# Performance work log

Measured on AMD Instinct MI355X. Metric: run time of the kernel, lower is better.

The kernel has to match this reference:

```python
import jax, jax.numpy as jnp
import numpy as np

DIM = 1024
HID = 256
MAXT = 2048
B = 4
T = 2048


def setup_inputs() -> dict:
    key = jax.random.key(0)
    ks = jax.random.split(key, 10)
    s_in = 1.0 / np.sqrt(DIM)   # keeps K ~ N(0,1) so exp(K) is stable
    s_h = 1.0 / np.sqrt(HID)
    # xavier-uniform bound for square wbias: sqrt(6/(T+T))
    wb_bound = float(np.sqrt(6.0 / (MAXT + MAXT)))
    return {
        "x": jax.random.normal(ks[0], (B, T, DIM), dtype=jnp.float32),
        "Wq": jax.random.normal(ks[1], (DIM, HID), dtype=jnp.float32) * s_in,
        "bq": jnp.zeros((HID,), dtype=jnp.float32),
        "Wk": jax.random.normal(ks[2], (DIM, HID), dtype=jnp.float32) * s_in,
        "bk": jnp.zeros((HID,), dtype=jnp.float32),
        "Wv": jax.random.normal(ks[3], (DIM, HID), dtype=jnp.float32) * s_in,
        "bv": jnp.zeros((HID,), dtype=jnp.float32),
        "Wp": jax.random.normal(ks[4], (HID, DIM), dtype=jnp.float32) * s_h,
        "bp": jnp.zeros((DIM,), dtype=jnp.float32),
        "wbias": jax.random.uniform(ks[5], (MAXT, MAXT), dtype=jnp.float32,
                                    minval=-wb_bound, maxval=wb_bound),
    }


def reference(x, Wq, bq, Wk, bk, Wv, bv, Wp, bp, wbias):
    Bn, Tn, _ = x.shape
    Q = x @ Wq + bq            # [B,T,H]
    K = x @ Wk + bk            # [B,T,H]
    V = x @ Wv + bv            # [B,T,H]
    ew = jnp.exp(wbias[:Tn, :Tn])          # [T,T]
    eK = jnp.exp(K)                         # [B,T,H]
    num = jnp.einsum('ts,bsh->bth', ew, eK * V)   # [B,T,H]
    den = jnp.einsum('ts,bsh->bth', ew, eK)       # [B,T,H]
    Yt = jax.nn.sigmoid(Q) * (num / den)          # [B,T,H]
    return Yt @ Wp + bp                            # [B,T,DIM]
```

## Files before the change

### kernel.cpp

```cpp
#include <hip/hip_runtime.h>
#include <hip/hip_bf16.h>


typedef __attribute__((ext_vector_type(8))) short bf16x8;
typedef __attribute__((ext_vector_type(4))) float f32x4;

static __device__ __forceinline__ unsigned short f2b(float f) {
  __hip_bfloat16 h = __float2bfloat16(f);
  return __builtin_bit_cast(unsigned short, h);
}

static __device__ __forceinline__ void gld16(const void* g, const void* l) {
  __builtin_amdgcn_global_load_lds((const __attribute__((address_space(1))) void*)g,
                                   (__attribute__((address_space(3))) void*)l, 16, 0, 0);
}

static __device__ __forceinline__ void gemm_loop(
    const unsigned short* __restrict__ A_blk,
    const unsigned short* __restrict__ Bt_blk,
    int K, int nk, char* AsB, char* BsB, f32x4 acc[4][2],
    int tid, int wr, int wc, int fr, int fkb)
{
  const int srow = tid >> 2;
  const int sk   = (tid & 3) * 8;
  const unsigned short* ap0 = A_blk + (long)srow * K + sk;
  const unsigned short* ap1 = ap0 + 64 * (long)K;
  const unsigned short* bp0 = Bt_blk + (long)srow * K + sk;

  gld16(ap0, AsB + tid * 16);
  gld16(ap1, AsB + 4096 + tid * 16);
  gld16(bp0, BsB + tid * 16);
  ap0 += 32; ap1 += 32; bp0 += 32;
  __syncthreads();

  int buf = 0;
  for (int kt = 0; kt < nk; ++kt) {
    if (kt + 1 < nk) {
      char* nA = AsB + ((buf ^ 1) << 13) + tid * 16;
      char* nB = BsB + ((buf ^ 1) << 12) + tid * 16;
      gld16(ap0, nA);
      gld16(ap1, nA + 4096);
      gld16(bp0, nB);
      ap0 += 32; ap1 += 32; bp0 += 32;
    }
    const char* Ab = AsB + (buf << 13);
    const char* Bb = BsB + (buf << 12);
    bf16x8 av[4], bv[2];
#pragma unroll
    for (int m = 0; m < 4; ++m)
      av[m] = *(const bf16x8*)(Ab + (wr * 64 + m * 16 + fr) * 64 + fkb);
#pragma unroll
    for (int n = 0; n < 2; ++n)
      bv[n] = *(const bf16x8*)(Bb + (wc * 32 + n * 16 + fr) * 64 + fkb);
#pragma unroll
    for (int m = 0; m < 4; ++m)
#pragma unroll
      for (int n = 0; n < 2; ++n)
        acc[m][n] = __builtin_amdgcn_mfma_f32_16x16x32_bf16(av[m], bv[n], acc[m][n], 0, 0, 0);
    __syncthreads();
    buf ^= 1;
  }
}

__global__ __launch_bounds__(256) void gemm1_qkv(
    const unsigned short* __restrict__ xb, const unsigned short* __restrict__ WqkvT,
    const float* __restrict__ biascat,
    float* __restrict__ sgQ, unsigned short* __restrict__ B2T)
{
  __shared__ char AsB[16384];
  __shared__ char BsB[8192];
  const int tid = threadIdx.x, lane = tid & 63, wave = tid >> 6;
  const int wr = wave >> 1, wc = wave & 1;
  const int fr = lane & 15, fkb = (lane >> 4) * 16, q4 = (lane >> 4) * 2 * 2;
  const long bm = (long)blockIdx.y * 128;
  const long bn = (long)blockIdx.x * 64;
  const int  b  = (int)(bm >> 11);
  const int  tb = (int)(bm & 2047);

  f32x4 acc[4][2] = {};
  gemm_loop(xb + bm * 1024, WqkvT + bn * 1024, 1024, 32, AsB, BsB, acc,
            tid, wr, wc, fr, fkb);

  if (bn < 256) {
#pragma unroll
    for (int n = 0; n < 2; ++n) {
      const int col = (int)bn + wc * 32 + n * 16 + fr;
      const float bb = biascat[col];
#pragma unroll
      for (int m = 0; m < 4; ++m) {
#pragma unroll
        for (int r = 0; r < 4; ++r) {
          long row = bm + wr * 64 + m * 16 + q4 + r;
          float v = acc[m][n][r] + bb;
          sgQ[row * 256 + col] = 1.f / (1.f + __expf(-v));
        }
      }
    }
  } else {
#pragma unroll
    for (int n = 0; n < 2; ++n) {
      const int col = (int)bn + wc * 32 + n * 16 + fr;
      const int u   = col - 256;
      const float bb = biascat[col];
      const bool isK = (u & 1) == 0;
      const long rw = (long)b * 512 + u + (isK ? 1 : -1);
#pragma unroll
      for (int m = 0; m < 4; ++m) {
        float v[4], o[4];
#pragma unroll
        for (int r = 0; r < 4; ++r) v[r] = acc[m][n][r] + bb;
#pragma unroll
        for (int r = 0; r < 4; ++r) o[r] = __shfl_xor(v[r], 1);
        ushort4 pk;
        if (isK) {
          pk.x = f2b(__expf(v[0])); pk.y = f2b(__expf(v[1]));
          pk.z = f2b(__expf(v[2])); pk.w = f2b(__expf(v[3]));
        } else {
          pk.x = f2b(__expf(o[0]) * v[0]); pk.y = f2b(__expf(o[1]) * v[1]);
          pk.z = f2b(__expf(o[2]) * v[2]); pk.w = f2b(__expf(o[3]) * v[3]);
        }
        const int t0 = tb + wr * 64 + m * 16 + q4;
        *(ushort4*)(B2T + rw * 2048 + t0) = pk;
      }
    }
  }
}

__global__ __launch_bounds__(256) void gemm2_aft(
    const unsigned short* __restrict__ ewb, const unsigned short* __restrict__ B2T,
    const float* __restrict__ sgQ, unsigned short* __restrict__ Yt)
{
  __shared__ char AsB[16384];
  __shared__ char BsB[8192];
  __shared__ float epi[128 * 32];
  const int tid = threadIdx.x, lane = tid & 63, wave = tid >> 6;
  const int wr = wave >> 1, wc = wave & 1;
  const int fr = lane & 15, fkb = (lane >> 4) * 16, q4 = (lane >> 4) * 2 * 2;
  const long bm = (long)blockIdx.y * 128;
  const long bn = (long)blockIdx.x * 64;
  const int  b  = (int)(bn >> 9);
  const int  h0 = (int)((bn & 511) >> 1);

  f32x4 acc[4][2] = {};
  gemm_loop(ewb + bm * 2048, B2T + bn * 2048, 2048, 64, AsB, BsB, acc,
            tid, wr, wc, fr, fkb);

  const bool even = (fr & 1) == 0;
#pragma unroll
  for (int n = 0; n < 2; ++n) {
    const int hl = wc * 16 + n * 8 + (fr >> 1);
#pragma unroll
    for (int m = 0; m < 4; ++m) {
#pragma unroll
      for (int r = 0; r < 4; ++r) {
        float own = acc[m][n][r];
        float oth = __shfl_xor(own, 1);
        if (even) {
          int tl = wr * 64 + m * 16 + q4 + r;
          epi[tl * 32 + hl] = own / oth;
        }
      }
    }
  }
  __syncthreads();

  const long mbase = (long)b * 2048 + bm;
#pragma unroll
  for (int p = 0; p < 16; ++p) {
    int row = p * 8 + (tid >> 5);
    int hl  = tid & 31;
    long mrow = mbase + row;
    int  hg   = h0 + hl;
    float v = epi[row * 32 + hl] * sgQ[mrow * 256 + hg];
    Yt[mrow * 256 + hg] = f2b(v);
  }
}

__global__ __launch_bounds__(256) void gemm_bt(
    const unsigned short* __restrict__ A, const unsigned short* __restrict__ Bt,
    float* __restrict__ C, const float* __restrict__ bias, int M, int N, int K)
{
  __shared__ char AsB[16384];
  __shared__ char BsB[8192];
  const int tid = threadIdx.x, lane = tid & 63, wave = tid >> 6;
  const int wr = wave >> 1, wc = wave & 1;
  const int fr = lane & 15, fkb = (lane >> 4) * 16, q4 = (lane >> 4) * 2 * 2;
  const long bm = (long)blockIdx.y * 128;
  const long bn = (long)blockIdx.x * 64;

  f32x4 acc[4][2] = {};
  gemm_loop(A + bm * (long)K, Bt + bn * (long)K, K, K >> 5, AsB, BsB, acc,
            tid, wr, wc, fr, fkb);

  const long crow0 = bm + wr * 64 + q4;
  const long ccol0 = bn + wc * 32 + fr;
#pragma unroll
  for (int n = 0; n < 2; ++n) {
    const long col = ccol0 + n * 16;
    const float bb = bias ? bias[col] : 0.f;
#pragma unroll
    for (int m = 0; m < 4; ++m)
#pragma unroll
      for (int r = 0; r < 4; ++r)
        C[(crow0 + m * 16 + r) * (long)N + col] = acc[m][n][r] + bb;
  }
}

__global__ void prep_kernel(const float* __restrict__ x, const float* __restrict__ wbias,
                            const float* __restrict__ Wq, const float* __restrict__ Wk,
                            const float* __restrict__ Wv, const float* __restrict__ bq,
                            const float* __restrict__ bk, const float* __restrict__ bv,
                            const float* __restrict__ Wp,
                            unsigned short* __restrict__ xb, unsigned short* __restrict__ ewb,
                            unsigned short* __restrict__ WqkvT, unsigned short* __restrict__ WpT,
                            float* __restrict__ biascat) {
  const int bid = blockIdx.x;
  const int t = threadIdx.x;
  if (bid < 8192) {
    int i = bid * 256 + t;
    float4 v = ((const float4*)x)[i];
    ushort4 o; o.x = f2b(v.x); o.y = f2b(v.y); o.z = f2b(v.z); o.w = f2b(v.w);
    ((ushort4*)xb)[i] = o;
  } else if (bid < 12288) {
    int i = (bid - 8192) * 256 + t;
    float4 v = ((const float4*)wbias)[i];
    ushort4 o;
    o.x = f2b(__expf(v.x)); o.y = f2b(__expf(v.y));
    o.z = f2b(__expf(v.z)); o.w = f2b(__expf(v.w));
    ((ushort4*)ewb)[i] = o;
  } else {
    int idx = (bid - 12288) * 256 + t;
    if (idx < 768 * 1024) {
      int n = idx >> 10, k = idx & 1023;
      const float* W; int c;
      if (n < 256) { W = Wq; c = n; }
      else { int u = n - 256; c = u >> 1; W = (u & 1) ? Wv : Wk; }
      WqkvT[idx] = f2b(W[k * 256 + c]);
    }
    if (idx < 1024 * 256) {
      int d = idx >> 8, h = idx & 255;
      WpT[idx] = f2b(Wp[h * 1024 + d]);
    }
    if (idx < 768) {
      float v;
      if (idx < 256) v = bq[idx];
      else { int u = idx - 256; v = (u & 1) ? bv[u >> 1] : bk[u >> 1]; }
      biascat[idx] = v;
    }
  }
}

extern "C" void kernel_launch(void* const* d_in, const int* in_sizes, int n_in,
                              void* d_out, int out_size, void* d_ws, size_t ws_size,
                              hipStream_t stream) {
  const float* x     = (const float*)d_in[0];
  const float* Wq    = (const float*)d_in[1];
  const float* bq    = (const float*)d_in[2];
  const float* Wk    = (const float*)d_in[3];
  const float* bk    = (const float*)d_in[4];
  const float* Wv    = (const float*)d_in[5];
  const float* bv    = (const float*)d_in[6];
  const float* Wp    = (const float*)d_in[7];
  const float* bp    = (const float*)d_in[8];
  const float* wbias = (const float*)d_in[9];

  char* ws = (char*)d_ws;
  unsigned short* xb      = (unsigned short*)(ws + 0);
  unsigned short* ewb     = (unsigned short*)(ws + 16777216);
  unsigned short* WqkvT   = (unsigned short*)(ws + 25165824);
  unsigned short* WpT     = (unsigned short*)(ws + 26738688);
  float*          biascat = (float*)(ws + 27262976);
  float*          sgQ     = (float*)(ws + 27267072);
  unsigned short* B2T     = (unsigned short*)(ws + 35655680);
  unsigned short* Yt      = (unsigned short*)(ws + 44044288);
  float* out = (float*)d_out;

  prep_kernel<<<15360, 256, 0, stream>>>(x, wbias, Wq, Wk, Wv, bq, bk, bv, Wp,
                                         xb, ewb, WqkvT, WpT, biascat);
  gemm1_qkv<<<dim3(12, 64), 256, 0, stream>>>(xb, WqkvT, biascat, sgQ, B2T);
  gemm2_aft<<<dim3(32, 16), 256, 0, stream>>>(ewb, B2T, sgQ, Yt);
  gemm_bt<<<dim3(16, 64), 256, 0, stream>>>(Yt, WpT, out, bp, 8192, 1024, 256);
}
```

Before: 199.8 us.

## Switch GEMMs to 128x128 tiles and split-K the AFT GEMM with a reduce kernel

All GEMMs now use 128x128 block tiles with a 4x4 MFMA accumulator per wave, replacing 128x64. The inner loop drops double buffering for a single buffer with a full vmcnt wait. The AFT GEMM becomes a generic split-K gemm_bt that writes fp32 partial slices, sized by available workspace. A new elementwise kernel sums the slices, divides num by den and multiplies by sigmoid(Q). The aim is more reuse per tile and more parallelism for the 2048-deep GEMM, at the cost of an extra fp32 round trip, an extra launch and lost load/compute overlap.

```diff
diff --git a/kernel.cpp b/kernel.cpp
--- a/kernel.cpp
+++ b/kernel.cpp
@@ -15,50 +15,78 @@
                                    (__attribute__((address_space(3))) void*)l, 16, 0, 0);
 }
 
-static __device__ __forceinline__ void gemm_loop(
+static __device__ __forceinline__ void core128(
     const unsigned short* __restrict__ A_blk,
     const unsigned short* __restrict__ Bt_blk,
-    int K, int nk, char* AsB, char* BsB, f32x4 acc[4][2],
+    long sA, long sB, int nk, char* AsB, char* BsB, f32x4 acc[4][4],
     int tid, int wr, int wc, int fr, int fkb)
 {
   const int srow = tid >> 2;
   const int sk   = (tid & 3) * 8;
-  const unsigned short* ap0 = A_blk + (long)srow * K + sk;
-  const unsigned short* ap1 = ap0 + 64 * (long)K;
-  const unsigned short* bp0 = Bt_blk + (long)srow * K + sk;
-
-  gld16(ap0, AsB + tid * 16);
-  gld16(ap1, AsB + 4096 + tid * 16);
-  gld16(bp0, BsB + tid * 16);
-  ap0 += 32; ap1 += 32; bp0 += 32;
-  __syncthreads();
-
-  int buf = 0;
+  const unsigned short* ap0 = A_blk + (long)srow * sA + sk;
+  const unsigned short* ap1 = ap0 + 64 * sA;
+  const unsigned short* bp0 = Bt_blk + (long)srow * sB + sk;
+  const unsigned short* bp1 = bp0 + 64 * sB;
+  char* la0 = AsB + tid * 16;
+  char* la1 = AsB + 4096 + tid * 16;
+  char* lb0 = BsB + tid * 16;
+  char* lb1 = BsB + 4096 + tid * 16;
+
   for (int kt = 0; kt < nk; ++kt) {
-    if (kt + 1 < nk) {
-      char* nA = AsB + ((buf ^ 1) << 13) + tid * 16;
-      char* nB = BsB + ((buf ^ 1) << 12) + tid * 16;
-      gld16(ap0, nA);
-      gld16(ap1, nA + 4096);
-      gld16(bp0, nB);
-      ap0 += 32; ap1 += 32; bp0 += 32;
-    }
-    const char* Ab = AsB + (buf << 13);
-    const char* Bb = BsB + (buf << 12);
-    bf16x8 av[4], bv[2];
+    gld16(ap0, la0);
+    gld16(ap1, la1);
+    gld16(bp0, lb0);
+    gld16(bp1, lb1);
+    ap0 += 32; ap1 += 32; bp0 += 32; bp1 += 32;
+    asm volatile("s_waitcnt vmcnt(0)" ::: "memory");
+    __syncthreads();
+
+    bf16x8 av[4], bv[4];
 #pragma unroll
     for (int m = 0; m < 4; ++m)
-      av[m] = *(const bf16x8*)(Ab + (wr * 64 + m * 16 + fr) * 64 + fkb);
-#pragma unroll
-    for (int n = 0; n < 2; ++n)
-      bv[n] = *(const bf16x8*)(Bb + (wc * 32 + n * 16 + fr) * 64 + fkb);
+      av[m] = *(const bf16x8*)(AsB + (wr * 64 + m * 16 + fr) * 64 + fkb);
+#pragma unroll
+    for (int n = 0; n < 4; ++n)
+      bv[n] = *(const bf16x8*)(BsB + (wc * 64 + n * 16 + fr) * 64 + fkb);
 #pragma unroll
     for (int m = 0; m < 4; ++m)
 #pragma unroll
-      for (int n = 0; n < 2; ++n)
+      for (int n = 0; n < 4; ++n)
         acc[m][n] = __builtin_amdgcn_mfma_f32_16x16x32_bf16(av[m], bv[n], acc[m][n], 0, 0, 0);
     __syncthreads();
-    buf ^= 1;
+  }
+}
+
+__global__ __launch_bounds__(256) void gemm_bt(
+    const unsigned short* __restrict__ A, const unsigned short* __restrict__ Bt,
+    float* __restrict__ C, const float* __restrict__ bias,
+    int M, int N, int K, int Ksub)
+{
+  __shared__ char AsB[8192];
+  __shared__ char BsB[8192];
+  const int tid = threadIdx.x, lane = tid & 63, wave = tid >> 6;
+  const int wr = wave >> 1, wc = wave & 1;
+  const int fr = lane & 15, fkb = (lane >> 4) * 16, q4 = (lane >> 4) * 4;
+  const long bm = (long)blockIdx.y * 128;
+  const long bn = (long)blockIdx.x * 128;
+  const long k0 = (long)blockIdx.z * Ksub;
+
+  f32x4 acc[4][4] = {};
+  core128(A + bm * K + k0, Bt + bn * K + k0, K, K, Ksub >> 5,
+          AsB, BsB, acc, tid, wr, wc, fr, fkb);
+
+  float* Cz = C + (long)blockIdx.z * M * (long)N;
+  const long crow0 = bm + wr * 64 + q4;
+  const long ccol0 = bn + wc * 64 + fr;
+#pragma unroll
+  for (int n = 0; n < 4; ++n) {
+    const long col = ccol0 + n * 16;
+    const float bb = bias ? bias[col] : 0.f;
+#pragma unroll
+    for (int m = 0; m < 4; ++m)
+#pragma unroll
+      for (int r = 0; r < 4; ++r)
+        Cz[(crow0 + m * 16 + r) * (long)N + col] = acc[m][n][r] + bb;
   }
 }
 
@@ -67,39 +95,38 @@
     const float* __restrict__ biascat,
     float* __restrict__ sgQ, unsigned short* __restrict__ B2T)
 {
-  __shared__ char AsB[16384];
+  __shared__ char AsB[8192];
   __shared__ char BsB[8192];
   const int tid = threadIdx.x, lane = tid & 63, wave = tid >> 6;
   const int wr = wave >> 1, wc = wave & 1;
-  const int fr = lane & 15, fkb = (lane >> 4) * 16, q4 = (lane >> 4) * 2 * 2;
+  const int fr = lane & 15, fkb = (lane >> 4) * 16, q4 = (lane >> 4) * 4;
   const long bm = (long)blockIdx.y * 128;
-  const long bn = (long)blockIdx.x * 64;
+  const long bn = (long)blockIdx.x * 128;
   const int  b  = (int)(bm >> 11);
   const int  tb = (int)(bm & 2047);
 
-  f32x4 acc[4][2] = {};
-  gemm_loop(xb + bm * 1024, WqkvT + bn * 1024, 1024, 32, AsB, BsB, acc,
-            tid, wr, wc, fr, fkb);
+  f32x4 acc[4][4] = {};
+  core128(xb + bm * 1024, WqkvT + bn * 1024, 1024, 1024, 32,
+          AsB, BsB, acc, tid, wr, wc, fr, fkb);
 
   if (bn < 256) {
 #pragma unroll
-    for (int n = 0; n < 2; ++n) {
-      const int col = (int)bn + wc * 32 + n * 16 + fr;
+    for (int n = 0; n < 4; ++n) {
+      const int col = (int)bn + wc * 64 + n * 16 + fr;
       const float bb = biascat[col];
 #pragma unroll
-      for (int m = 0; m < 4; ++m) {
+      for (int m = 0; m < 4; ++m)
 #pragma unroll
         for (int r = 0; r < 4; ++r) {
           long row = bm + wr * 64 + m * 16 + q4 + r;
           float v = acc[m][n][r] + bb;
           sgQ[row * 256 + col] = 1.f / (1.f + __expf(-v));
         }
-      }
     }
   } else {
 #pragma unroll
-    for (int n = 0; n < 2; ++n) {
-      const int col = (int)bn + wc * 32 + n * 16 + fr;
+    for (int n = 0; n < 4; ++n) {
+      const int col = (int)bn + wc * 64 + n * 16 + fr;
       const int u   = col - 256;
       const float bb = biascat[col];
       const bool isK = (u & 1) == 0;
@@ -126,84 +153,19 @@
   }
 }
 
-__global__ __launch_bounds__(256) void gemm2_aft(
-    const unsigned short* __restrict__ ewb, const unsigned short* __restrict__ B2T,
-    const float* __restrict__ sgQ, unsigned short* __restrict__ Yt)
-{
-  __shared__ char AsB[16384];
-  __shared__ char BsB[8192];
-  __shared__ float epi[128 * 32];
-  const int tid = threadIdx.x, lane = tid & 63, wave = tid >> 6;
-  const int wr = wave >> 1, wc = wave & 1;
-  const int fr = lane & 15, fkb = (lane >> 4) * 16, q4 = (lane >> 4) * 2 * 2;
-  const long bm = (long)blockIdx.y * 128;
-  const long bn = (long)blockIdx.x * 64;
-  const int  b  = (int)(bn >> 9);
-  const int  h0 = (int)((bn & 511) >> 1);
-
-  f32x4 acc[4][2] = {};
-  gemm_loop(ewb + bm * 2048, B2T + bn * 2048, 2048, 64, AsB, BsB, acc,
-            tid, wr, wc, fr, fkb);
-
-  const bool even = (fr & 1) == 0;
-#pragma unroll
-  for (int n = 0; n < 2; ++n) {
-    const int hl = wc * 16 + n * 8 + (fr >> 1);
-#pragma unroll
-    for (int m = 0; m < 4; ++m) {
-#pragma unroll
-      for (int r = 0; r < 4; ++r) {
-        float own = acc[m][n][r];
-        float oth = __shfl_xor(own, 1);
-        if (even) {
-          int tl = wr * 64 + m * 16 + q4 + r;
-          epi[tl * 32 + hl] = own / oth;
-        }
-      }
-    }
-  }
-  __syncthreads();
-
-  const long mbase = (long)b * 2048 + bm;
-#pragma unroll
-  for (int p = 0; p < 16; ++p) {
-    int row = p * 8 + (tid >> 5);
-    int hl  = tid & 31;
-    long mrow = mbase + row;
-    int  hg   = h0 + hl;
-    float v = epi[row * 32 + hl] * sgQ[mrow * 256 + hg];
-    Yt[mrow * 256 + hg] = f2b(v);
-  }
-}
-
-__global__ __launch_bounds__(256) void gemm_bt(
-    const unsigned short* __restrict__ A, const unsigned short* __restrict__ Bt,
-    float* __restrict__ C, const float* __restrict__ bias, int M, int N, int K)
-{
-  __shared__ char AsB[16384];
-  __shared__ char BsB[8192];
-  const int tid = threadIdx.x, lane = tid & 63, wave = tid >> 6;
-  const int wr = wave >> 1, wc = wave & 1;
-  const int fr = lane & 15, fkb = (lane >> 4) * 16, q4 = (lane >> 4) * 2 * 2;
-  const long bm = (long)blockIdx.y * 128;
-  const long bn = (long)blockIdx.x * 64;
-
-  f32x4 acc[4][2] = {};
-  gemm_loop(A + bm * (long)K, Bt + bn * (long)K, K, K >> 5, AsB, BsB, acc,
-            tid, wr, wc, fr, fkb);
-
-  const long crow0 = bm + wr * 64 + q4;
-  const long ccol0 = bn + wc * 32 + fr;
-#pragma unroll
-  for (int n = 0; n < 2; ++n) {
-    const long col = ccol0 + n * 16;
-    const float bb = bias ? bias[col] : 0.f;
-#pragma unroll
-    for (int m = 0; m < 4; ++m)
-#pragma unroll
-      for (int r = 0; r < 4; ++r)
-        C[(crow0 + m * 16 + r) * (long)N + col] = acc[m][n][r] + bb;
-  }
+__global__ void elt2_kernel(const float* __restrict__ C2, const float* __restrict__ sgQ,
+                            unsigned short* __restrict__ Yt, int nslices) {
+  int idx = blockIdx.x * 256 + threadIdx.x;
+  int h = idx & 255, m = idx >> 8;
+  int b = m >> 11, tt = m & 2047;
+  long p2 = ((long)tt * 2048 + b * 512) >> 1;
+  const float2* C22 = (const float2*)C2;
+  float num = 0.f, den = 0.f;
+  for (int z = 0; z < nslices; ++z) {
+    float2 nd = C22[(long)z * 2097152 + p2 + h];
+    num += nd.x; den += nd.y;
+  }
+  Yt[idx] = f2b(sgQ[idx] * num / den);
 }
 
 __global__ void prep_kernel(const float* __restrict__ x, const float* __restrict__ wbias,
@@ -264,20 +226,28 @@
   const float* bp    = (const float*)d_in[8];
   const float* wbias = (const float*)d_in[9];
 
+  int nslices = 1;
+  if (ws_size >= 4ull * 16777216 + 31461376) nslices = 4;
+  else if (ws_size >= 2ull * 16777216 + 31461376) nslices = 2;
+
   char* ws = (char*)d_ws;
+  const long base = (long)nslices * 16777216;
   unsigned short* xb      = (unsigned short*)(ws + 0);
-  unsigned short* ewb     = (unsigned short*)(ws + 16777216);
-  unsigned short* WqkvT   = (unsigned short*)(ws + 25165824);
-  unsigned short* WpT     = (unsigned short*)(ws + 26738688);
-  float*          biascat = (float*)(ws + 27262976);
-  float*          sgQ     = (float*)(ws + 27267072);
-  unsigned short* B2T     = (unsigned short*)(ws + 35655680);
-  unsigned short* Yt      = (unsigned short*)(ws + 44044288);
+  float*          C2      = (float*)(ws + 0);
+  unsigned short* ewb     = (unsigned short*)(ws + base);
+  unsigned short* WqkvT   = (unsigned short*)(ws + base + 8388608);
+  unsigned short* WpT     = (unsigned short*)(ws + base + 9961472);
+  float*          biascat = (float*)(ws + base + 10485760);
+  float*          sgQ     = (float*)(ws + base + 10489856);
+  unsigned short* B2T     = (unsigned short*)(ws + base + 18878464);
+  unsigned short* Yt      = (unsigned short*)(ws + base + 27267072);
   float* out = (float*)d_out;
 
   prep_kernel<<<15360, 256, 0, stream>>>(x, wbias, Wq, Wk, Wv, bq, bk, bv, Wp,
                                          xb, ewb, WqkvT, WpT, biascat);
-  gemm1_qkv<<<dim3(12, 64), 256, 0, stream>>>(xb, WqkvT, biascat, sgQ, B2T);
-  gemm2_aft<<<dim3(32, 16), 256, 0, stream>>>(ewb, B2T, sgQ, Yt);
-  gemm_bt<<<dim3(16, 64), 256, 0, stream>>>(Yt, WpT, out, bp, 8192, 1024, 256);
-}
+  gemm1_qkv<<<dim3(6, 64), 256, 0, stream>>>(xb, WqkvT, biascat, sgQ, B2T);
+  gemm_bt<<<dim3(16, 16, nslices), 256, 0, stream>>>(ewb, B2T, C2, nullptr,
+                                                     2048, 2048, 2048, 2048 / nslices);
+  elt2_kernel<<<8192, 256, 0, stream>>>(C2, sgQ, Yt, nslices);
+  gemm_bt<<<dim3(8, 64, 1), 256, 0, stream>>>(Yt, WpT, out, bp, 8192, 1024, 256, 256);
+}
```

Result: slower. 207.6 us (+3.9%).
